# Kernel optimization log

Measured on AMD Instinct MI355X. Metric: run time of the kernel, lower is better.

Reference implementation:

```python
import jax, jax.numpy as jnp
import numpy as np

# Model hyperparameters (match init_kwargs)
G = 256      # graph_size
K = 6        # conv kernel size
CH = 8       # channels
ROWS = 4
COLS = 3
B = 64       # batch
H = G - K + 1  # conv output side (square) = 251


def setup_inputs() -> dict:
    key = jax.random.key(0)
    k1, k2, k3, k4 = jax.random.split(key, 4)
    x = jax.random.normal(k1, (B, G, G), dtype=jnp.float32)
    # Conv2d(1, CH, (K,K)) weights, kaiming_normal_ (fan_in = 1*K*K, gain=sqrt(2))
    fan_in = 1 * K * K
    conv_w = jax.random.normal(k2, (CH, 1, K, K), dtype=jnp.float32) * np.float32(np.sqrt(2.0 / fan_in))
    # torch Conv2d default bias init: U(-1/sqrt(fan_in), 1/sqrt(fan_in))
    bound = np.float32(1.0 / np.sqrt(fan_in))
    conv_b = jax.random.uniform(k3, (CH,), dtype=jnp.float32, minval=-bound, maxval=bound)
    # coef parameter [CH, ROWS, COLS], kaiming_normal_ (fan_in = ROWS*COLS)
    coef = jax.random.normal(k4, (CH, ROWS, COLS), dtype=jnp.float32) * np.float32(np.sqrt(2.0 / (ROWS * COLS)))
    return {"x": x, "conv_w": conv_w, "conv_b": conv_b, "coef": coef}


def _traces_of_powers(C):
    """C: [H,H]. Returns traces of C^(i+2) for i in 0..ROWS-1 (matches torch loop:
    x_series[0]=C@C; at step i it records trace(x_series[i]) = trace(C^(i+2))."""
    def step(P, _):
        return C @ P, jnp.trace(P)
    _, ts = jax.lax.scan(step, C @ C, None, length=ROWS)
    return ts  # [ROWS]


def reference(x, conv_w, conv_b, coef):
    # conv over each sample treated as [1,1,G,G] -> vectorized as [B,1,G,G]
    y = jax.lax.conv_general_dilated(
        x[:, None], conv_w, window_strides=(1, 1), padding='VALID',
        dimension_numbers=('NCHW', 'OIHW', 'NCHW'))
    y = y + conv_b[None, :, None, None]           # [B, CH, H, H]

    ts = jax.vmap(jax.vmap(_traces_of_powers))(y)  # [B, CH, ROWS]

    jpow = jnp.arange(1, COLS + 1, dtype=jnp.float32)            # exponents j+1
    ret = ts[..., None] ** jpow                                  # [B, CH, ROWS, COLS]
    numel = jnp.float32(H * H)
    exps = (jnp.arange(ROWS, dtype=jnp.float32)[:, None]
            + jnp.arange(COLS, dtype=jnp.float32)[None, :] + 1.0)  # i+j+1
    ret = ret / (numel ** exps)                                  # [B, CH, ROWS, COLS]

    terms = coef[None] * ret
    return terms.sum(axis=(1, 2, 3))  # [B]
```

## Files before the change

kernel.cpp:

```cpp
#include <hip/hip_runtime.h>

typedef short short8 __attribute__((ext_vector_type(8)));
typedef float f32x4 __attribute__((ext_vector_type(4)));

#define B_    64
#define CH_   8
#define NBC   512
#define MATU  65536
#define H_    251
#define PADX  73
#define LDSW  40

__device__ inline unsigned short bf16r(float f){
    unsigned u = __float_as_uint(f);
    u += 0x7fffu + ((u >> 16) & 1u);
    return (unsigned short)(u >> 16);
}
__device__ inline float bf16f(unsigned short h){ return __uint_as_float(((unsigned)h) << 16); }
__device__ inline unsigned packsplit(float v){
    unsigned short h = bf16r(v);
    unsigned short l = bf16r(v - bf16f(h));
    return (((unsigned)h) << 16) | (unsigned)l;
}
__device__ inline float unpackf(unsigned u){
    return __uint_as_float(u & 0xffff0000u) + bf16f((unsigned short)(u & 0xffffu));
}

__global__ __launch_bounds__(256) void conv_pack(const float* __restrict__ x,
                                                 const float* __restrict__ w,
                                                 const float* __restrict__ bias,
                                                 unsigned* __restrict__ Ypk,
                                                 int b_base) {
    __shared__ float xt[69 * PADX];
    __shared__ float wsm[148];

    int tid = threadIdx.x;
    int tile = blockIdx.x;
    int lb = blockIdx.y;
    int cq = blockIdx.z;
    int b = b_base + lb;
    int r0 = (tile >> 2) * 64, c0 = (tile & 3) * 64;

    if (tid < 144) wsm[tid] = w[cq * 144 + tid];
    if (tid < 4)   wsm[144 + tid] = bias[cq * 4 + tid];

    const float* xb = x + (size_t)b * 65536;
    for (int idx = tid; idx < 69 * PADX; idx += 256) {
        int row = idx / PADX, col = idx - row * PADX;
        float v = 0.f;
        if (col < 69) {
            int gr = r0 + row; if (gr > 255) gr = 255;
            int gc = c0 + col; if (gc > 255) gc = 255;
            v = xb[gr * 256 + gc];
        }
        xt[idx] = v;
    }
    __syncthreads();

    int tx = tid & 15, ty = tid >> 4;

    float acc[4][4][4];
    #pragma unroll
    for (int cc = 0; cc < 4; ++cc) {
        float bv = wsm[144 + cc];
        #pragma unroll
        for (int i = 0; i < 4; ++i)
            #pragma unroll
            for (int j = 0; j < 4; ++j) acc[cc][i][j] = bv;
    }

    #pragma unroll
    for (int ir = 0; ir < 9; ++ir) {
        float row[9];
        #pragma unroll
        for (int c = 0; c < 9; ++c) row[c] = xt[(ty * 4 + ir) * PADX + tx * 4 + c];
        #pragma unroll
        for (int cc = 0; cc < 4; ++cc) {
            const float* wc = &wsm[cc * 36];
            #pragma unroll
            for (int i = 0; i < 4; ++i) {
                int u = ir - i;
                if (u >= 0 && u < 6) {
                    #pragma unroll
                    for (int v = 0; v < 6; ++v) {
                        float wv = wc[u * 6 + v];
                        #pragma unroll
                        for (int j = 0; j < 4; ++j) acc[cc][i][j] += row[j + v] * wv;
                    }
                }
            }
        }
    }

    #pragma unroll
    for (int cc = 0; cc < 4; ++cc) {
        int ch = cq * 4 + cc;
        unsigned pk[4][4];
        #pragma unroll
        for (int i = 0; i < 4; ++i) {
            int gr = r0 + ty * 4 + i;
            #pragma unroll
            for (int j = 0; j < 4; ++j) {
                int gc = c0 + tx * 4 + j;
                float v = (gr < H_ && gc < H_) ? acc[cc][i][j] : 0.f;
                pk[i][j] = packsplit(v);
            }
        }
        unsigned* yrow = Ypk + (size_t)(lb * 8 + ch) * MATU;
        #pragma unroll
        for (int i = 0; i < 4; ++i) {
            uint4 v = make_uint4(pk[i][0], pk[i][1], pk[i][2], pk[i][3]);
            *(uint4*)&yrow[(size_t)(r0 + ty * 4 + i) * 256 + c0 + tx * 4] = v;
        }
    }
}

template<int PHASE>
__global__ __launch_bounds__(256, 4) void gemm_mfma(const unsigned* __restrict__ Apk,
                                                    const unsigned* __restrict__ Ypk,
                                                    unsigned* __restrict__ Mpk,
                                                    double* __restrict__ pdiag,
                                                    double* __restrict__ pfull,
                                                    int bc_base, int cur) {
    __shared__ __align__(16) char smem[36864];
    __shared__ double redbuf[8];

    unsigned short* Ahi = (unsigned short*)smem;
    unsigned short* Alo = (unsigned short*)(smem + 10240);
    unsigned short* Bhi = (unsigned short*)(smem + 20480);
    unsigned short* Blo = (unsigned short*)(smem + 28672);

    int tid = threadIdx.x;

    int hw = blockIdx.x;
    int xcd = hw & 7, s = hw >> 3;
    int mpx = cur >> 3;
    int lbc = xcd * mpx + (s >> 2);
    int t4 = s & 3;
    int by = t4 >> 1, bx = t4 & 1;
    int bi = by * 128, bj = bx * 128;
    int bc = bc_base + lbc;

    const unsigned* A = Apk + (size_t)lbc * MATU;

    int wid = tid >> 6, l = tid & 63;
    int wr = wid >> 1, wc = wid & 1;
    int l15 = l & 15, lk = l >> 4;

    f32x4 acc[4][4];
    #pragma unroll
    for (int m = 0; m < 4; ++m)
        #pragma unroll
        for (int n = 0; n < 4; ++n) acc[m][n] = (f32x4){0.f, 0.f, 0.f, 0.f};

    const int cl  = tid & 31;
    const int grp = tid >> 5;
    const int kq  = grp * 4;
    const int kb  = grp >> 1;
    const int koff = (grp & 1) * 4;

    for (int k0 = 0; k0 < 256; k0 += 32) {
        #pragma unroll
        for (int p = 0; p < 4; ++p) {
            int g = p * 256 + tid;
            int row = g >> 3, chn = g & 7;
            uint4 qa = *(const uint4*)(A + (size_t)(bi + row) * 256 + k0 + chn * 4);
            *(ushort4*)&Ahi[row * LDSW + chn * 4] =
                make_ushort4(qa.x >> 16, qa.y >> 16, qa.z >> 16, qa.w >> 16);
            *(ushort4*)&Alo[row * LDSW + chn * 4] =
                make_ushort4(qa.x & 0xffff, qa.y & 0xffff, qa.z & 0xffff, qa.w & 0xffff);
        }
        {
            const unsigned* Bp = A + (size_t)(k0 + kq) * 256 + bj + cl;
            unsigned d[4][4];
            #pragma unroll
            for (int i = 0; i < 4; ++i)
                #pragma unroll
                for (int j = 0; j < 4; ++j)
                    d[i][j] = Bp[i * 256 + j * 32];
            #pragma unroll
            for (int j = 0; j < 4; ++j) {
                int c = cl + 32 * j;
                *(ushort4*)&Bhi[kb * 1024 + c * 8 + koff] =
                    make_ushort4(d[0][j] >> 16, d[1][j] >> 16, d[2][j] >> 16, d[3][j] >> 16);
                *(ushort4*)&Blo[kb * 1024 + c * 8 + koff] =
                    make_ushort4(d[0][j] & 0xffff, d[1][j] & 0xffff, d[2][j] & 0xffff, d[3][j] & 0xffff);
            }
        }
        __syncthreads();

        short8 ah[4], al[4], bh[4], bl[4];
        #pragma unroll
        for (int m = 0; m < 4; ++m) {
            int r = wr * 64 + m * 16 + l15;
            ah[m] = *(const short8*)&Ahi[r * LDSW + lk * 8];
            al[m] = *(const short8*)&Alo[r * LDSW + lk * 8];
        }
        #pragma unroll
        for (int n = 0; n < 4; ++n) {
            int c = wc * 64 + n * 16 + l15;
            bh[n] = *(const short8*)&Bhi[lk * 1024 + c * 8];
            bl[n] = *(const short8*)&Blo[lk * 1024 + c * 8];
        }
        #pragma unroll
        for (int m = 0; m < 4; ++m)
            #pragma unroll
            for (int n = 0; n < 4; ++n) {
                acc[m][n] = __builtin_amdgcn_mfma_f32_16x16x32_bf16(ah[m], bh[n], acc[m][n], 0, 0, 0);
                acc[m][n] = __builtin_amdgcn_mfma_f32_16x16x32_bf16(ah[m], bl[n], acc[m][n], 0, 0, 0);
                acc[m][n] = __builtin_amdgcn_mfma_f32_16x16x32_bf16(al[m], bh[n], acc[m][n], 0, 0, 0);
            }
        __syncthreads();
    }

    const unsigned* Yb = Ypk + (size_t)lbc * MATU;
    unsigned* Mw = (PHASE == 1) ? (Mpk + (size_t)lbc * MATU) : nullptr;
    float s_full = 0.f, s_diag = 0.f;
    #pragma unroll
    for (int m = 0; m < 4; ++m) {
        int rg0 = bi + wr * 64 + m * 16 + lk * 4;
        #pragma unroll
        for (int n = 0; n < 4; ++n) {
            int cg = bj + wc * 64 + n * 16 + l15;
            uint4 yq = *(const uint4*)(Yb + (size_t)cg * 256 + rg0);
            unsigned yu[4] = {yq.x, yq.y, yq.z, yq.w};
            f32x4 v = acc[m][n];
            #pragma unroll
            for (int reg = 0; reg < 4; ++reg) {
                float val = v[reg];
                s_full += val * unpackf(yu[reg]);
                if (rg0 + reg == cg) s_diag += val;
                if (PHASE == 1) Mw[(size_t)(rg0 + reg) * 256 + cg] = packsplit(val);
            }
        }
    }

    double df = (double)s_full, dd = (double)s_diag;
    #pragma unroll
    for (int off = 32; off > 0; off >>= 1) {
        df += __shfl_down(df, off, 64);
        dd += __shfl_down(dd, off, 64);
    }
    __syncthreads();
    if (l == 0) { redbuf[wid] = df; redbuf[4 + wid] = dd; }
    __syncthreads();
    if (tid == 0) {
        pfull[(size_t)bc * 4 + by * 2 + bx] =
            redbuf[0] + redbuf[1] + redbuf[2] + redbuf[3];
        if (bx == by)
            pdiag[(size_t)bc * 2 + bx] =
                redbuf[4] + redbuf[5] + redbuf[6] + redbuf[7];
    }
}

__global__ void combine(const double* __restrict__ p2, const double* __restrict__ p3,
                        const double* __restrict__ p4, const double* __restrict__ p5,
                        const float* __restrict__ coef, float* __restrict__ out) {
    int b = threadIdx.x;
    if (b >= B_) return;
    const double numel = (double)(H_ * H_);
    double acc = 0.0;
    for (int ch = 0; ch < CH_; ++ch) {
        int bc = b * CH_ + ch;
        double t[4];
        t[0] = p2[bc * 2] + p2[bc * 2 + 1];
        t[1] = p3[bc * 4] + p3[bc * 4 + 1] + p3[bc * 4 + 2] + p3[bc * 4 + 3];
        t[2] = p4[bc * 2] + p4[bc * 2 + 1];
        t[3] = p5[bc * 4] + p5[bc * 4 + 1] + p5[bc * 4 + 2] + p5[bc * 4 + 3];
        double npow_i = numel;
        for (int i = 0; i < 4; ++i) {
            double tv = t[i];
            double p = tv, d = npow_i;
            for (int j = 0; j < 3; ++j) {
                acc += (double)coef[ch * 12 + i * 3 + j] * (p / d);
                p *= tv;
                d *= numel;
            }
            npow_i *= numel;
        }
    }
    out[b] = (float)acc;
}

extern "C" void kernel_launch(void* const* d_in, const int* in_sizes, int n_in,
                              void* d_out, int out_size, void* d_ws, size_t ws_size,
                              hipStream_t stream) {
    const float* x    = (const float*)d_in[0];
    const float* w    = (const float*)d_in[1];
    const float* bias = (const float*)d_in[2];
    const float* coef = (const float*)d_in[3];
    float* out = (float*)d_out;

    double* p2 = (double*)d_ws;
    double* p3 = p2 + NBC * 2;
    double* p4 = p3 + NBC * 4;
    double* p5 = p4 + NBC * 2;
    const size_t head = 65536;

    const size_t per_mat = (size_t)MATU * 4;
    size_t avail = (ws_size > head) ? ws_size - head : 0;
    int NC = (int)(avail / (2 * per_mat));
    NC &= ~7;
    if (NC > 256) NC = 256;
    if (NC < 8) NC = 8;

    unsigned* Ypk = (unsigned*)((char*)d_ws + head);
    unsigned* Mpk = Ypk + (size_t)NC * MATU;

    for (int bc0 = 0; bc0 < NBC; bc0 += NC) {
        int cur = NBC - bc0;
        if (cur > NC) cur = NC;
        int nb = cur / 8;
        conv_pack<<<dim3(16, nb, 2), 256, 0, stream>>>(x, w, bias, Ypk, bc0 / 8);
        gemm_mfma<1><<<cur * 4, 256, 0, stream>>>(Ypk, Ypk, Mpk, p2, p3, bc0, cur);
        gemm_mfma<2><<<cur * 4, 256, 0, stream>>>(Mpk, Ypk, nullptr, p4, p5, bc0, cur);
    }
    combine<<<1, 64, 0, stream>>>(p2, p3, p4, p5, coef, out);
}
```

Baseline: 242.0 us.

## Double-buffer B tile in LDS, prefetch via registers, load A fragments directly

The GEMM main loop now double-buffers the B tile in shared memory and prefetches the next K-slice of B into registers while the current slice is consumed, which removes the second barrier per iteration. The A operand is no longer staged through LDS: each lane reads its MFMA fragment straight from global memory and splits it into hi/lo bf16 in registers. This cuts LDS traffic and synchronisation, but A fragments are re-read from global/L2 by both column-warps with strided per-lane loads, which can raise cache traffic and latency.

```diff
diff --git a/kernel.cpp b/kernel.cpp
--- a/kernel.cpp
+++ b/kernel.cpp
@@ -9,7 +9,6 @@
 #define MATU  65536
 #define H_    251
 #define PADX  73
-#define LDSW  40
 
 __device__ inline unsigned short bf16r(float f){
     unsigned u = __float_as_uint(f);
@@ -25,6 +24,8 @@
 __device__ inline float unpackf(unsigned u){
     return __uint_as_float(u & 0xffff0000u) + bf16f((unsigned short)(u & 0xffffu));
 }
+
+union U4H8 { uint4 q[2]; unsigned u[8]; };
 
 __global__ __launch_bounds__(256) void conv_pack(const float* __restrict__ x,
                                                  const float* __restrict__ w,
@@ -122,13 +123,9 @@
                                                     double* __restrict__ pdiag,
                                                     double* __restrict__ pfull,
                                                     int bc_base, int cur) {
-    __shared__ __align__(16) char smem[36864];
+    __shared__ __align__(16) unsigned short BhiS[2][4096];
+    __shared__ __align__(16) unsigned short BloS[2][4096];
     __shared__ double redbuf[8];
-
-    unsigned short* Ahi = (unsigned short*)smem;
-    unsigned short* Alo = (unsigned short*)(smem + 10240);
-    unsigned short* Bhi = (unsigned short*)(smem + 20480);
-    unsigned short* Blo = (unsigned short*)(smem + 28672);
 
     int tid = threadIdx.x;
 
@@ -159,42 +156,50 @@
     const int kb  = grp >> 1;
     const int koff = (grp & 1) * 4;
 
-    for (int k0 = 0; k0 < 256; k0 += 32) {
-        #pragma unroll
-        for (int p = 0; p < 4; ++p) {
-            int g = p * 256 + tid;
-            int row = g >> 3, chn = g & 7;
-            uint4 qa = *(const uint4*)(A + (size_t)(bi + row) * 256 + k0 + chn * 4);
-            *(ushort4*)&Ahi[row * LDSW + chn * 4] =
-                make_ushort4(qa.x >> 16, qa.y >> 16, qa.z >> 16, qa.w >> 16);
-            *(ushort4*)&Alo[row * LDSW + chn * 4] =
-                make_ushort4(qa.x & 0xffff, qa.y & 0xffff, qa.z & 0xffff, qa.w & 0xffff);
-        }
-        {
-            const unsigned* Bp = A + (size_t)(k0 + kq) * 256 + bj + cl;
-            unsigned d[4][4];
+    unsigned d[4][4];
+    {
+        const unsigned* Bp = A + (size_t)kq * 256 + bj + cl;
+        #pragma unroll
+        for (int i = 0; i < 4; ++i)
+            #pragma unroll
+            for (int j = 0; j < 4; ++j)
+                d[i][j] = Bp[i * 256 + j * 32];
+    }
+
+    for (int ks = 0; ks < 8; ++ks) {
+        unsigned short* Bhi = BhiS[ks & 1];
+        unsigned short* Blo = BloS[ks & 1];
+        #pragma unroll
+        for (int j = 0; j < 4; ++j) {
+            int c = cl + 32 * j;
+            *(ushort4*)&Bhi[kb * 1024 + c * 8 + koff] =
+                make_ushort4(d[0][j] >> 16, d[1][j] >> 16, d[2][j] >> 16, d[3][j] >> 16);
+            *(ushort4*)&Blo[kb * 1024 + c * 8 + koff] =
+                make_ushort4(d[0][j] & 0xffff, d[1][j] & 0xffff, d[2][j] & 0xffff, d[3][j] & 0xffff);
+        }
+        if (ks < 7) {
+            const unsigned* Bp = A + (size_t)((ks + 1) * 32 + kq) * 256 + bj + cl;
             #pragma unroll
             for (int i = 0; i < 4; ++i)
                 #pragma unroll
                 for (int j = 0; j < 4; ++j)
                     d[i][j] = Bp[i * 256 + j * 32];
-            #pragma unroll
-            for (int j = 0; j < 4; ++j) {
-                int c = cl + 32 * j;
-                *(ushort4*)&Bhi[kb * 1024 + c * 8 + koff] =
-                    make_ushort4(d[0][j] >> 16, d[1][j] >> 16, d[2][j] >> 16, d[3][j] >> 16);
-                *(ushort4*)&Blo[kb * 1024 + c * 8 + koff] =
-                    make_ushort4(d[0][j] & 0xffff, d[1][j] & 0xffff, d[2][j] & 0xffff, d[3][j] & 0xffff);
-            }
         }
         __syncthreads();
 
+        int k0 = ks * 32;
         short8 ah[4], al[4], bh[4], bl[4];
         #pragma unroll
         for (int m = 0; m < 4; ++m) {
-            int r = wr * 64 + m * 16 + l15;
-            ah[m] = *(const short8*)&Ahi[r * LDSW + lk * 8];
-            al[m] = *(const short8*)&Alo[r * LDSW + lk * 8];
+            const unsigned* ap = A + (size_t)(bi + wr * 64 + m * 16 + l15) * 256 + k0 + lk * 8;
+            U4H8 q;
+            q.q[0] = *(const uint4*)(ap);
+            q.q[1] = *(const uint4*)(ap + 4);
+            unsigned short hv[8], lv[8];
+            #pragma unroll
+            for (int e = 0; e < 8; ++e) { hv[e] = q.u[e] >> 16; lv[e] = q.u[e] & 0xffff; }
+            ah[m] = *(short8*)hv;
+            al[m] = *(short8*)lv;
         }
         #pragma unroll
         for (int n = 0; n < 4; ++n) {
@@ -210,7 +215,6 @@
                 acc[m][n] = __builtin_amdgcn_mfma_f32_16x16x32_bf16(ah[m], bl[n], acc[m][n], 0, 0, 0);
                 acc[m][n] = __builtin_amdgcn_mfma_f32_16x16x32_bf16(al[m], bh[n], acc[m][n], 0, 0, 0);
             }
-        __syncthreads();
     }
 
     const unsigned* Yb = Ypk + (size_t)lbc * MATU;
```

Measured after the change: 447.6 us. 1.85x slower.
